# Performance work log

Measured on AMD Instinct MI355X. Metric: run time of the kernel, lower is better.

Reference implementation:

```python
import jax, jax.numpy as jnp
import numpy as np

B, QL, KL, D, H = 2, 512, 8192, 1024, 8
HD = D // H  # head dim = 128


def setup_inputs() -> dict:
    key = jax.random.key(0)
    ks = jax.random.split(key, 12)
    s = 0.02
    return {
        "inputs_q": jax.random.normal(ks[0], (B, QL, D), jnp.float32),
        "inputs_k": jax.random.normal(ks[1], (B, KL, D), jnp.float32),
        "inputs_v": jax.random.normal(ks[2], (B, KL, D), jnp.float32),
        "attention_mask": jax.random.randint(ks[3], (B, QL, KL), 0, 2).astype(bool),
        "Wq": jax.random.normal(ks[4], (D, D), jnp.float32) * s,
        "bq": jnp.zeros((D,), jnp.float32),
        "Wk": jax.random.normal(ks[5], (D, D), jnp.float32) * s,
        "bk": jnp.zeros((D,), jnp.float32),
        "Wv": jax.random.normal(ks[6], (D, D), jnp.float32) * s,
        "bv": jnp.zeros((D,), jnp.float32),
        "Wf": jax.random.normal(ks[7], (D, D), jnp.float32) * s,
        "bf": jnp.zeros((D,), jnp.float32),
    }


def reference(inputs_q, inputs_k, inputs_v, attention_mask, Wq, bq, Wk, bk, Wv, bv, Wf, bf):
    # Projections (torch Linear: x @ W.T + b)
    q = inputs_q @ Wq.T + bq  # [B, QL, D]
    k = inputs_k @ Wk.T + bk  # [B, KL, D]
    v = inputs_v @ Wv.T + bv  # [B, KL, D]

    q = q.reshape(B, QL, H, HD)
    k = k.reshape(B, KL, H, HD)
    v = v.reshape(B, KL, H, HD)

    # scores [B, H, QL, KL]
    scores = jnp.einsum("bqhd,bkhd->bhqk", q, k)
    scale = 1.0 / np.sqrt(HD).astype(np.float32)
    scores = scores * scale
    large_k = jnp.float32(1e30)
    scores = jnp.where(attention_mask[:, None, :, :], scores, -large_k)

    probs = jax.nn.softmax(scores, axis=-1)
    # note: original calls self.dropout(normalized) but discards the result -> no-op

    summed = jnp.einsum("bhqk,bkhd->bqhd", probs, v).reshape(B, QL, H * HD)

    # wipe rows whose mask is all zero
    wipe = jnp.all(~attention_mask, axis=2, keepdims=True)  # [B, QL, 1]
    summed = jnp.where(wipe, jnp.zeros_like(summed), summed)

    return summed @ Wf.T + bf
```

## Files before the change

kernel.cpp:

```cpp
#include <hip/hip_runtime.h>
#include <hip/hip_bf16.h>
#include <math.h>

typedef __attribute__((ext_vector_type(4))) float fx4;
typedef __attribute__((ext_vector_type(4))) short sx4;
typedef __attribute__((ext_vector_type(8))) short sx8;
typedef unsigned long long u64;

#define MFMA16(a, b, c) __builtin_amdgcn_mfma_f32_16x16x16bf16_1k(a, b, c, 0, 0, 0)
#define MFMA32(a, b, c) __builtin_amdgcn_mfma_f32_16x16x32_bf16(a, b, c, 0, 0, 0)

__device__ __forceinline__ unsigned short f2bf(float f) {
  unsigned int u = __float_as_uint(f);
  return (unsigned short)((u + 0x7fffu + ((u >> 16) & 1u)) >> 16);
}

__device__ __forceinline__ unsigned cvtpk(float lo, float hi) {
  unsigned r;
  asm("v_cvt_pk_bf16_f32 %0, %1, %2" : "=v"(r) : "v"(lo), "v"(hi));
  return r;
}

typedef const __attribute__((address_space(1))) char* gc1p;
typedef __attribute__((address_space(3))) char* lc3p;
__device__ __forceinline__ void glds16(const void* g, const void* lds_uniform) {
  gc1p gp = (gc1p)(unsigned long long)(uintptr_t)g;
  lc3p lp = (lc3p)(unsigned)__builtin_amdgcn_readfirstlane((int)(unsigned)(uintptr_t)lds_uniform);
  __builtin_amdgcn_global_load_lds(gp, lp, 16, 0, 0);
}

__global__ __launch_bounds__(256) void k_prep(
    const float* __restrict__ Wq, const float* __restrict__ Wk,
    const float* __restrict__ Wv, const float* __restrict__ Wf,
    const int* __restrict__ mask, short* cwq, short* cwk, short* cwv,
    short* cwf, u64* __restrict__ mb) {
  __shared__ unsigned char nib[4][256];
  const int bx = blockIdx.x;
  const int t = threadIdx.x;
  if (bx >= 256) {
    const int mrow0 = (bx - 256) * 4;
#pragma unroll
    for (int j = 0; j < 4; j++) {
      const int4 m = *(const int4*)(mask + (size_t)(mrow0 + j) * 1024 + t * 4);
      nib[j][t] = (unsigned char)((m.x != 0) | ((m.y != 0) << 1) |
                                  ((m.z != 0) << 2) | ((m.w != 0) << 3));
    }
    __syncthreads();
    if (t < 64) {
      const int j = t >> 4, i = t & 15;
      u64 wv = 0;
#pragma unroll
      for (int k = 0; k < 16; k++)
        wv |= (u64)(nib[j][i * 16 + k] & 0xF) << (4 * k);
      mb[(size_t)(mrow0 + j) * 16 + i] = wv;
    }
    return;
  }
  const int seg = bx >> 6;
  const float* s = seg == 0 ? Wq : seg == 1 ? Wk : seg == 2 ? Wv : Wf;
  short* d = seg == 0 ? cwq : seg == 1 ? cwk : seg == 2 ? cwv : cwf;
  const size_t base = (size_t)(bx & 63) * 16384;
#pragma unroll
  for (int it = 0; it < 4; it++) {
    const size_t i = base + (size_t)it * 4096 + (size_t)t * 16;
    const fx4 a0 = *(const fx4*)(s + i);
    const fx4 a1 = *(const fx4*)(s + i + 4);
    const fx4 a2 = *(const fx4*)(s + i + 8);
    const fx4 a3 = *(const fx4*)(s + i + 12);
    sx8 o0, o1;
    o0[0] = (short)f2bf(a0[0]); o0[1] = (short)f2bf(a0[1]);
    o0[2] = (short)f2bf(a0[2]); o0[3] = (short)f2bf(a0[3]);
    o0[4] = (short)f2bf(a1[0]); o0[5] = (short)f2bf(a1[1]);
    o0[6] = (short)f2bf(a1[2]); o0[7] = (short)f2bf(a1[3]);
    o1[0] = (short)f2bf(a2[0]); o1[1] = (short)f2bf(a2[1]);
    o1[2] = (short)f2bf(a2[2]); o1[3] = (short)f2bf(a2[3]);
    o1[4] = (short)f2bf(a3[0]); o1[5] = (short)f2bf(a3[1]);
    o1[6] = (short)f2bf(a3[2]); o1[7] = (short)f2bf(a3[3]);
    *(sx8*)(d + i) = o0;
    *(sx8*)(d + i + 8) = o1;
  }
}

template <int MODE, int MT, int AF32>
__device__ __forceinline__ void gemm_body(short* sA, short* sB,
                                          const void* __restrict__ Aptr,
                                          const short* __restrict__ Bw,
                                          const float* __restrict__ bias,
                                          void* __restrict__ Cptr, int M, int N,
                                          int K, float alpha, int bx) {
  const int t = threadIdx.x;
  const int lane = t & 63;
  const int w = t >> 6;
  const int quad = lane >> 4;
  const int l16 = lane & 15;
  const int x7 = l16 & 7;
  int m0, n0;
  if (M >= 8192) {
    const int ml = bx & 7, nn = (bx >> 3) & 7, mh = bx >> 6;
    m0 = (mh * 8 + ml) * MT;
    n0 = nn << 7;
  } else {
    const int ntile = N >> 7;
    n0 = (bx % ntile) << 7;
    m0 = (bx / ntile) * MT;
  }
  constexpr int NI = (MT == 128) ? 4 : 2;
  constexpr int NJ = (MT == 128) ? 4 : 2;
  const int wm = (MT == 128) ? ((w >> 1) << 6) : 0;
  const int wn = (MT == 128) ? ((w & 1) << 6) : (w << 5);
  const fx4 fzero = {0.f, 0.f, 0.f, 0.f};
  fx4 acc[4][NI];
#pragma unroll
  for (int i = 0; i < 4; i++)
#pragma unroll
    for (int j = 0; j < NI; j++) acc[i][j] = fzero;

  const int srow = lane >> 3;
  const int scb = lane & 7;
  const float* Af = (const float*)Aptr;
  const short* Ab = (const short*)Aptr;
  fx4 ra[NJ][2];

  if (AF32) {
#pragma unroll
    for (int j = 0; j < NJ; j++) {
      const int rbase = (MT == 128) ? (w * 32 + j * 8) : (j * 32 + w * 8);
      const int row = rbase + srow;
      const int cb = scb ^ (row & 7);
      const float* src = Af + (size_t)(m0 + row) * K + cb * 8;
      ra[j][0] = *(const fx4*)src;
      ra[j][1] = *(const fx4*)(src + 4);
    }
  }

  for (int k0 = 0; k0 < K; k0 += 64) {
    __syncthreads();
    if (AF32) {
#pragma unroll
      for (int j = 0; j < NJ; j++) {
        const int rbase = (MT == 128) ? (w * 32 + j * 8) : (j * 32 + w * 8);
        sx8 o;
        unsigned* ou = (unsigned*)&o;
        ou[0] = cvtpk(ra[j][0][0], ra[j][0][1]);
        ou[1] = cvtpk(ra[j][0][2], ra[j][0][3]);
        ou[2] = cvtpk(ra[j][1][0], ra[j][1][1]);
        ou[3] = cvtpk(ra[j][1][2], ra[j][1][3]);
        *(sx8*)(&sA[rbase * 64 + lane * 8]) = o;
      }
    } else {
#pragma unroll
      for (int j = 0; j < NJ; j++) {
        const int rbase = (MT == 128) ? (w * 32 + j * 8) : (j * 32 + w * 8);
        const int row = rbase + srow;
        const int cb = scb ^ (row & 7);
        glds16(Ab + (size_t)(m0 + row) * K + k0 + cb * 8, &sA[rbase * 64]);
      }
    }
#pragma unroll
    for (int j = 0; j < 4; j++) {
      const int row = w * 32 + j * 8 + srow;
      const int cb = scb ^ (row & 7);
      glds16(Bw + (size_t)(n0 + row) * K + k0 + cb * 8, &sB[(w * 32 + j * 8) * 64]);
    }
    __syncthreads();
    if (AF32 && k0 + 64 < K) {
#pragma unroll
      for (int j = 0; j < NJ; j++) {
        const int rbase = (MT == 128) ? (w * 32 + j * 8) : (j * 32 + w * 8);
        const int row = rbase + srow;
        const int cb = scb ^ (row & 7);
        const float* src = Af + (size_t)(m0 + row) * K + (k0 + 64) + cb * 8;
        ra[j][0] = *(const fx4*)src;
        ra[j][1] = *(const fx4*)(src + 4);
      }
    }
#pragma unroll
    for (int kc = 0; kc < 2; kc++) {
      const int cbp = ((kc * 4 + quad) ^ x7) * 8;
      sx8 fa[4], fb[NI];
#pragma unroll
      for (int i = 0; i < 4; i++)
        fa[i] = *(const sx8*)(&sA[(wm + i * 16 + l16) * 64 + cbp]);
#pragma unroll
      for (int i = 0; i < NI; i++)
        fb[i] = *(const sx8*)(&sB[(wn + i * 16 + l16) * 64 + cbp]);
#pragma unroll
      for (int mi = 0; mi < 4; mi++)
#pragma unroll
        for (int ni = 0; ni < NI; ni++)
          acc[mi][ni] = MFMA32(fa[mi], fb[ni], acc[mi][ni]);
    }
  }
#pragma unroll
  for (int ni = 0; ni < NI; ni++) {
    const int col = n0 + wn + ni * 16 + l16;
    const float bval = bias[col];
    if (MODE == 2) {
#pragma unroll
      for (int mi = 0; mi < 4; mi++) {
        const int rowb = m0 + wm + mi * 16 + quad * 4;
        const int bb = rowb >> 13;
        const int kl = (rowb & 8191) ^ ((col & 8) ? 4 : 0);
        sx4 pkv;
#pragma unroll
        for (int r = 0; r < 4; r++) pkv[r] = (short)f2bf(acc[mi][ni][r] + bval);
        *(sx4*)((unsigned short*)Cptr + ((size_t)bb * 1024 + col) * 8192 + kl) = pkv;
      }
    } else {
#pragma unroll
      for (int mi = 0; mi < 4; mi++)
#pragma unroll
        for (int r = 0; r < 4; r++) {
          const int row = m0 + wm + mi * 16 + quad * 4 + r;
          const float v = (acc[mi][ni][r] + bval) * alpha;
          if (MODE == 1) ((float*)Cptr)[(size_t)row * N + col] = v;
          else ((unsigned short*)Cptr)[(size_t)row * N + col] = f2bf(v);
        }
    }
  }
}

__global__ __launch_bounds__(256) void k_gemm_k(const float* __restrict__ ink,
                                                const short* __restrict__ cwk,
                                                const float* __restrict__ bk,
                                                short* __restrict__ Kp) {
  __shared__ __align__(16) short smem[16384];
  gemm_body<0, 128, 1>(smem, smem + 8192, ink, cwk, bk, Kp, 16384, 1024, 1024,
                       1.f, blockIdx.x);
}

__global__ __launch_bounds__(256) void k_proj_vq(
    const float* __restrict__ inv, const short* __restrict__ cwv,
    const float* __restrict__ bv, short* __restrict__ Vt,
    const float* __restrict__ inq, const short* __restrict__ cwq,
    const float* __restrict__ bq, short* __restrict__ Qp, float alpha_q) {
  __shared__ __align__(16) short smem[16384];
  const int bx = blockIdx.x;
  if (bx < 128)
    gemm_body<0, 64, 1>(smem, smem + 8192, inq, cwq, bq, Qp, 1024, 1024, 1024,
                        alpha_q, bx);
  else
    gemm_body<2, 128, 1>(smem, smem + 8192, inv, cwv, bv, Vt, 16384, 1024, 1024,
                         1.f, bx - 128);
}

__global__ __launch_bounds__(256) void k_gemm_out(const short* __restrict__ summed,
                                                  const short* __restrict__ cwf,
                                                  const float* __restrict__ bf,
                                                  float* __restrict__ out) {
  __shared__ __align__(16) short smem[16384];
  gemm_body<1, 64, 0>(smem, smem + 8192, summed, cwf, bf, out, 1024, 1024, 1024,
                      1.f, blockIdx.x);
}

__global__ __launch_bounds__(256, 4) void k_attn(const short* __restrict__ Qp,
                                                 const short* __restrict__ Kp,
                                                 const short* __restrict__ Vt,
                                                 const u64* __restrict__ mb,
                                                 float* __restrict__ ml,
                                                 float* __restrict__ Op) {
  __shared__ __align__(16) short sK[8192];
  __shared__ __align__(16) short sV[8192];
  const int x = blockIdx.x;
  const int gl = x & 7;
  const int qt = (x >> 3) & 7;
  const int gh = x >> 6;
  const int g = gh * 8 + gl;
  const int s = g & 7;
  const int h = (g >> 3) & 7;
  const int b = g >> 6;
  const int li = ((b * 8 + h) * 8 + qt) * 8 + s;
  const int t = threadIdx.x;
  const int lane = t & 63;
  const int w = t >> 6;
  const int quad = lane >> 4;
  const int l16 = lane & 15;
  const int x7 = l16 & 7;
  const int q0 = qt << 6;
  const fx4 fzero = {0.f, 0.f, 0.f, 0.f};

  const short* qbase = Qp + (size_t)(b * 512 + q0 + w * 16 + l16) * 1024 + h * 128;
  sx8 aq[4];
#pragma unroll
  for (int kc = 0; kc < 4; kc++) aq[kc] = *(const sx8*)(qbase + kc * 32 + quad * 8);

  fx4 Ot[8];
#pragma unroll
  for (int d = 0; d < 8; d++) Ot[d] = fzero;
  float lsum = 0.f;

  const short* kbase = Kp + (size_t)(b * 8192 + s * 1024) * 1024 + h * 128;
  const short* vbase = Vt + (size_t)(b * 1024 + h * 128) * 8192 + s * 1024;
  const u64* wdp = mb + (size_t)(b * 512 + q0 + w * 16 + l16) * 128 + s * 16;
  const int srow4 = lane >> 4, scb16 = lane & 15;
  const int srow8 = lane >> 3, scb8 = lane & 7;
  const int h4 = ((quad & 1) ^ ((l16 >> 3) & 1)) * 4;

  for (int kt = 0; kt < 16; kt++) {
    __syncthreads();
#pragma unroll
    for (int j = 0; j < 4; j++) {
      const int row = (w * 4 + j) * 4 + srow4;
      const int cb = scb16 ^ (row & 7);
      glds16(kbase + (size_t)(kt * 64 + row) * 1024 + cb * 8, &sK[(w * 4 + j) * 512]);
    }
#pragma unroll
    for (int j = 0; j < 4; j++) {
      const int row = (w * 4 + j) * 8 + srow8;
      const int cb = scb8 ^ (row & 7);
      glds16(vbase + (size_t)row * 8192 + kt * 64 + cb * 8, &sV[(w * 4 + j) * 512]);
    }
    const u64 wd = wdp[kt];
    __syncthreads();
    const unsigned lo = (unsigned)wd, hi = (unsigned)(wd >> 32);
    sx4 pk[4];
#pragma unroll
    for (int nt = 0; nt < 4; nt++) {
      fx4 a = fzero;
#pragma unroll
      for (int kc = 0; kc < 4; kc++) {
        const sx8 kf = *(const sx8*)(&sK[(nt * 16 + l16) * 128 + ((kc * 4 + quad) ^ x7) * 8]);
        a = MFMA32(kf, aq[kc], a);
      }
      const unsigned bits = (nt & 2) ? hi : lo;
      const int sh = (nt & 1) * 16 + quad * 4;
      float pv[4];
#pragma unroll
      for (int r = 0; r < 4; r++) {
        const float e = __builtin_amdgcn_exp2f(a[r]);
        pv[r] = ((bits >> (sh + r)) & 1u) ? e : 0.f;
        lsum += pv[r];
      }
      sx4 pko;
      ((unsigned*)&pko)[0] = __builtin_amdgcn_perm(
          __float_as_uint(pv[1]) + 0x8000u, __float_as_uint(pv[0]) + 0x8000u, 0x07060302u);
      ((unsigned*)&pko)[1] = __builtin_amdgcn_perm(
          __float_as_uint(pv[3]) + 0x8000u, __float_as_uint(pv[2]) + 0x8000u, 0x07060302u);
      pk[nt] = pko;
    }
#pragma unroll
    for (int dt = 0; dt < 8; dt++) {
      fx4 o = Ot[dt];
#pragma unroll
      for (int nt = 0; nt < 4; nt++) {
        const int cb = (2 * nt + (quad >> 1)) ^ x7;
        const sx4 vf = *(const sx4*)(&sV[(dt * 16 + l16) * 64 + cb * 8 + h4]);
        o = MFMA16(vf, pk[nt], o);
      }
      Ot[dt] = o;
    }
  }
  lsum += __shfl_xor(lsum, 16, 64);
  lsum += __shfl_xor(lsum, 32, 64);
  if (lane < 16) ml[(size_t)li * 64 + w * 16 + l16] = lsum;
  float* ob = Op + (size_t)li * 8192 + (w * 16 + l16) * 128 + quad * 4;
#pragma unroll
  for (int dt = 0; dt < 8; dt++) *(fx4*)(ob + dt * 16) = Ot[dt];
}

__global__ __launch_bounds__(256) void k_combine(const float* __restrict__ ml,
                                                 const float* __restrict__ Op,
                                                 short* __restrict__ summed) {
  const int bx = blockIdx.x;
  const int xc = bx >> 1;
  const int dh = (bx & 1) * 64;
  const int qt = xc & 7;
  const int h = (xc >> 3) & 7;
  const int b = xc >> 6;
  const int t = threadIdx.x;
  const int row = t >> 2;
  const int dg = dh + (t & 3) * 16;
  float L = 0.f;
#pragma unroll
  for (int s = 0; s < 8; s++) L += ml[(size_t)(xc * 8 + s) * 64 + row];
  float o[16];
#pragma unroll
  for (int i = 0; i < 16; i++) o[i] = 0.f;
  if (L != 0.f) {
#pragma unroll
    for (int s = 0; s < 8; s++) {
      const float* src = Op + (size_t)(xc * 8 + s) * 8192 + row * 128 + dg;
#pragma unroll
      for (int i = 0; i < 4; i++) {
        const fx4 v = *(const fx4*)(src + i * 4);
        o[i * 4 + 0] += v[0]; o[i * 4 + 1] += v[1];
        o[i * 4 + 2] += v[2]; o[i * 4 + 3] += v[3];
      }
    }
    const float inv = 1.f / L;
#pragma unroll
    for (int i = 0; i < 16; i++) o[i] *= inv;
  }
  short* dst = summed + (size_t)(b * 512 + qt * 64 + row) * 1024 + h * 128 + dg;
#pragma unroll
  for (int i = 0; i < 2; i++) {
    sx8 pkv;
#pragma unroll
    for (int j = 0; j < 8; j++) pkv[j] = (short)f2bf(o[i * 8 + j]);
    *(sx8*)(dst + i * 8) = pkv;
  }
}

extern "C" void kernel_launch(void* const* d_in, const int* in_sizes, int n_in,
                              void* d_out, int out_size, void* d_ws, size_t ws_size,
                              hipStream_t stream) {
  (void)in_sizes; (void)n_in; (void)out_size; (void)ws_size;
  const float* inq = (const float*)d_in[0];
  const float* ink = (const float*)d_in[1];
  const float* inv = (const float*)d_in[2];
  const int* mask = (const int*)d_in[3];
  const float* Wq = (const float*)d_in[4];
  const float* bq = (const float*)d_in[5];
  const float* Wk = (const float*)d_in[6];
  const float* bk = (const float*)d_in[7];
  const float* Wv = (const float*)d_in[8];
  const float* bv = (const float*)d_in[9];
  const float* Wf = (const float*)d_in[10];
  const float* bf = (const float*)d_in[11];

  char* ws = (char*)d_ws;
  short* Vt = (short*)(ws + 0);
  short* Kp = (short*)(ws + 33554432);
  float* Op = (float*)(ws + 67108864);
  short* cwq = (short*)(ws + 102760448);
  short* cwk = (short*)(ws + 104857600);
  short* cwv = (short*)(ws + 106954752);
  short* cwf = (short*)(ws + 109051904);
  short* Qp = (short*)(ws + 111149056);
  short* summed = (short*)(ws + 113246208);
  u64* mb = (u64*)(ws + 115343360);
  float* ml = (float*)(ws + 116391936);

  const float alpha_q = 0.12751757f;

  k_prep<<<2304, 256, 0, stream>>>(Wq, Wk, Wv, Wf, mask, cwq, cwk, cwv, cwf, mb);
  k_gemm_k<<<1024, 256, 0, stream>>>(ink, cwk, bk, Kp);
  k_proj_vq<<<1152, 256, 0, stream>>>(inv, cwv, bv, Vt, inq, cwq, bq, Qp, alpha_q);
  k_attn<<<1024, 256, 0, stream>>>(Qp, Kp, Vt, mb, ml, Op);
  k_combine<<<256, 256, 0, stream>>>(ml, Op, summed);
  k_gemm_out<<<128, 256, 0, stream>>>(summed, cwf, bf, (float*)d_out);
}
```

Measured before the change: 387.1 us.

## Double-buffer LDS in GEMM main loop and merge K/V/Q projection launches

The GEMM body now keeps two LDS buffers for A and B. It prefetches the next k-tile with async global-to-LDS loads and fp32 register loads while MFMAs run on the current tile, which drops one barrier per iteration. The separate K-projection and V/Q-projection kernels are merged into a single 2176-block launch, removing a launch boundary and a tail. In exchange, LDS per block doubles to 64 KB, which may lower occupancy.

```diff
diff --git a/kernel.cpp b/kernel.cpp
--- a/kernel.cpp
+++ b/kernel.cpp
@@ -131,11 +131,88 @@
       ra[j][0] = *(const fx4*)src;
       ra[j][1] = *(const fx4*)(src + 4);
     }
-  }
-
+  } else {
+#pragma unroll
+    for (int j = 0; j < NJ; j++) {
+      const int rbase = (MT == 128) ? (w * 32 + j * 8) : (j * 32 + w * 8);
+      const int row = rbase + srow;
+      const int cb = scb ^ (row & 7);
+      glds16(Ab + (size_t)(m0 + row) * K + cb * 8, &sA[rbase * 64]);
+    }
+  }
+#pragma unroll
+  for (int j = 0; j < 4; j++) {
+    const int row = w * 32 + j * 8 + srow;
+    const int cb = scb ^ (row & 7);
+    glds16(Bw + (size_t)(n0 + row) * K + cb * 8, &sB[(w * 32 + j * 8) * 64]);
+  }
+  if (AF32) {
+#pragma unroll
+    for (int j = 0; j < NJ; j++) {
+      const int rbase = (MT == 128) ? (w * 32 + j * 8) : (j * 32 + w * 8);
+      sx8 o;
+      unsigned* ou = (unsigned*)&o;
+      ou[0] = cvtpk(ra[j][0][0], ra[j][0][1]);
+      ou[1] = cvtpk(ra[j][0][2], ra[j][0][3]);
+      ou[2] = cvtpk(ra[j][1][0], ra[j][1][1]);
+      ou[3] = cvtpk(ra[j][1][2], ra[j][1][3]);
+      *(sx8*)(&sA[rbase * 64 + lane * 8]) = o;
+    }
+  }
+  __syncthreads();
+
+  int buf = 0;
   for (int k0 = 0; k0 < K; k0 += 64) {
-    __syncthreads();
-    if (AF32) {
+    const int nb = buf ^ 1;
+    const bool more = (k0 + 64 < K);
+    if (more) {
+#pragma unroll
+      for (int j = 0; j < 4; j++) {
+        const int row = w * 32 + j * 8 + srow;
+        const int cb = scb ^ (row & 7);
+        glds16(Bw + (size_t)(n0 + row) * K + (k0 + 64) + cb * 8,
+               &sB[nb * 8192 + (w * 32 + j * 8) * 64]);
+      }
+      if (AF32) {
+#pragma unroll
+        for (int j = 0; j < NJ; j++) {
+          const int rbase = (MT == 128) ? (w * 32 + j * 8) : (j * 32 + w * 8);
+          const int row = rbase + srow;
+          const int cb = scb ^ (row & 7);
+          const float* src = Af + (size_t)(m0 + row) * K + (k0 + 64) + cb * 8;
+          ra[j][0] = *(const fx4*)src;
+          ra[j][1] = *(const fx4*)(src + 4);
+        }
+      } else {
+#pragma unroll
+        for (int j = 0; j < NJ; j++) {
+          const int rbase = (MT == 128) ? (w * 32 + j * 8) : (j * 32 + w * 8);
+          const int row = rbase + srow;
+          const int cb = scb ^ (row & 7);
+          glds16(Ab + (size_t)(m0 + row) * K + (k0 + 64) + cb * 8,
+                 &sA[nb * 8192 + rbase * 64]);
+        }
+      }
+    }
+    const short* pA = sA + buf * 8192;
+    const short* pB = sB + buf * 8192;
+#pragma unroll
+    for (int kc = 0; kc < 2; kc++) {
+      const int cbp = ((kc * 4 + quad) ^ x7) * 8;
+      sx8 fa[4], fb[NI];
+#pragma unroll
+      for (int i = 0; i < 4; i++)
+        fa[i] = *(const sx8*)(&pA[(wm + i * 16 + l16) * 64 + cbp]);
+#pragma unroll
+      for (int i = 0; i < NI; i++)
+        fb[i] = *(const sx8*)(&pB[(wn + i * 16 + l16) * 64 + cbp]);
+#pragma unroll
+      for (int mi = 0; mi < 4; mi++)
+#pragma unroll
+        for (int ni = 0; ni < NI; ni++)
+          acc[mi][ni] = MFMA32(fa[mi], fb[ni], acc[mi][ni]);
+    }
+    if (AF32 && more) {
 #pragma unroll
       for (int j = 0; j < NJ; j++) {
         const int rbase = (MT == 128) ? (w * 32 + j * 8) : (j * 32 + w * 8);
@@ -145,51 +222,11 @@
         ou[1] = cvtpk(ra[j][0][2], ra[j][0][3]);
         ou[2] = cvtpk(ra[j][1][0], ra[j][1][1]);
         ou[3] = cvtpk(ra[j][1][2], ra[j][1][3]);
-        *(sx8*)(&sA[rbase * 64 + lane * 8]) = o;
-      }
-    } else {
-#pragma unroll
-      for (int j = 0; j < NJ; j++) {
-        const int rbase = (MT == 128) ? (w * 32 + j * 8) : (j * 32 + w * 8);
-        const int row = rbase + srow;
-        const int cb = scb ^ (row & 7);
-        glds16(Ab + (size_t)(m0 + row) * K + k0 + cb * 8, &sA[rbase * 64]);
-      }
-    }
-#pragma unroll
-    for (int j = 0; j < 4; j++) {
-      const int row = w * 32 + j * 8 + srow;
-      const int cb = scb ^ (row & 7);
-      glds16(Bw + (size_t)(n0 + row) * K + k0 + cb * 8, &sB[(w * 32 + j * 8) * 64]);
+        *(sx8*)(&sA[nb * 8192 + rbase * 64 + lane * 8]) = o;
+      }
     }
     __syncthreads();
-    if (AF32 && k0 + 64 < K) {
-#pragma unroll
-      for (int j = 0; j < NJ; j++) {
-        const int rbase = (MT == 128) ? (w * 32 + j * 8) : (j * 32 + w * 8);
-        const int row = rbase + srow;
-        const int cb = scb ^ (row & 7);
-        const float* src = Af + (size_t)(m0 + row) * K + (k0 + 64) + cb * 8;
-        ra[j][0] = *(const fx4*)src;
-        ra[j][1] = *(const fx4*)(src + 4);
-      }
-    }
-#pragma unroll
-    for (int kc = 0; kc < 2; kc++) {
-      const int cbp = ((kc * 4 + quad) ^ x7) * 8;
-      sx8 fa[4], fb[NI];
-#pragma unroll
-      for (int i = 0; i < 4; i++)
-        fa[i] = *(const sx8*)(&sA[(wm + i * 16 + l16) * 64 + cbp]);
-#pragma unroll
-      for (int i = 0; i < NI; i++)
-        fb[i] = *(const sx8*)(&sB[(wn + i * 16 + l16) * 64 + cbp]);
-#pragma unroll
-      for (int mi = 0; mi < 4; mi++)
-#pragma unroll
-        for (int ni = 0; ni < NI; ni++)
-          acc[mi][ni] = MFMA32(fa[mi], fb[ni], acc[mi][ni]);
-    }
+    buf = nb;
   }
 #pragma unroll
   for (int ni = 0; ni < NI; ni++) {
@@ -220,37 +257,33 @@
   }
 }
 
-__global__ __launch_bounds__(256) void k_gemm_k(const float* __restrict__ ink,
-                                                const short* __restrict__ cwk,
-                                                const float* __restrict__ bk,
-                                                short* __restrict__ Kp) {
-  __shared__ __align__(16) short smem[16384];
-  gemm_body<0, 128, 1>(smem, smem + 8192, ink, cwk, bk, Kp, 16384, 1024, 1024,
-                       1.f, blockIdx.x);
-}
-
-__global__ __launch_bounds__(256) void k_proj_vq(
+__global__ __launch_bounds__(256) void k_proj(
+    const float* __restrict__ ink, const short* __restrict__ cwk,
+    const float* __restrict__ bk, short* __restrict__ Kp,
     const float* __restrict__ inv, const short* __restrict__ cwv,
     const float* __restrict__ bv, short* __restrict__ Vt,
     const float* __restrict__ inq, const short* __restrict__ cwq,
     const float* __restrict__ bq, short* __restrict__ Qp, float alpha_q) {
-  __shared__ __align__(16) short smem[16384];
+  __shared__ __align__(16) short smem[32768];
   const int bx = blockIdx.x;
-  if (bx < 128)
-    gemm_body<0, 64, 1>(smem, smem + 8192, inq, cwq, bq, Qp, 1024, 1024, 1024,
-                        alpha_q, bx);
+  if (bx < 1024)
+    gemm_body<0, 128, 1>(smem, smem + 16384, ink, cwk, bk, Kp, 16384, 1024,
+                         1024, 1.f, bx);
+  else if (bx < 2048)
+    gemm_body<2, 128, 1>(smem, smem + 16384, inv, cwv, bv, Vt, 16384, 1024,
+                         1024, 1.f, bx - 1024);
   else
-    gemm_body<2, 128, 1>(smem, smem + 8192, inv, cwv, bv, Vt, 16384, 1024, 1024,
-                         1.f, bx - 128);
+    gemm_body<0, 64, 1>(smem, smem + 16384, inq, cwq, bq, Qp, 1024, 1024, 1024,
+                        alpha_q, bx - 2048);
 }
 
 __global__ __launch_bounds__(256) void k_gemm_out(const short* __restrict__ summed,
                                                   const short* __restrict__ cwf,
                                                   const float* __restrict__ bf,
                                                   float* __restrict__ out) {
-  __shared__ __align__(16) short smem[16384];
-  gemm_body<1, 64, 0>(smem, smem + 8192, summed, cwf, bf, out, 1024, 1024, 1024,
-                      1.f, blockIdx.x);
+  __shared__ __align__(16) short smem[32768];
+  gemm_body<1, 64, 0>(smem, smem + 16384, summed, cwf, bf, out, 1024, 1024,
+                      1024, 1.f, blockIdx.x);
 }
 
 __global__ __launch_bounds__(256, 4) void k_attn(const short* __restrict__ Qp,
@@ -434,8 +467,8 @@
   const float alpha_q = 0.12751757f;
 
   k_prep<<<2304, 256, 0, stream>>>(Wq, Wk, Wv, Wf, mask, cwq, cwk, cwv, cwf, mb);
-  k_gemm_k<<<1024, 256, 0, stream>>>(ink, cwk, bk, Kp);
-  k_proj_vq<<<1152, 256, 0, stream>>>(inv, cwv, bv, Vt, inq, cwq, bq, Qp, alpha_q);
+  k_proj<<<2176, 256, 0, stream>>>(ink, cwk, bk, Kp, inv, cwv, bv, Vt, inq, cwq,
+                                   bq, Qp, alpha_q);
   k_attn<<<1024, 256, 0, stream>>>(Qp, Kp, Vt, mb, ml, Op);
   k_combine<<<256, 256, 0, stream>>>(ml, Op, summed);
   k_gemm_out<<<128, 256, 0, stream>>>(summed, cwf, bf, (float*)d_out);
```

Result: no change. 380.8 us (-1.6%).
